# Optimization experiments

Measured on AMD Instinct MI355X. Metric: run time of the kernel, lower is better.

The kernel has to match this reference:

```python
import jax, jax.numpy as jnp
import numpy as np

N = 100000   # num nodes
F = 256      # feat_data dim == args.feat_dim (required by concat shapes)
D = 32       # fixed neighbor count per node
B = 8192     # batch of node indices
NEG = 10     # neg_sample_size (hard-coded in module)


def setup_inputs() -> dict:
    key = jax.random.key(0)
    ks = jax.random.split(key, 9)
    feat_data = jax.random.normal(ks[0], (N, F), dtype=jnp.float32)
    # self.feats[i] = [degrees[i]] * feat_dim
    degrees = jax.random.randint(ks[1], (N,), 1, 64).astype(jnp.float32)
    feats = jnp.tile(degrees[:, None], (1, F))
    W1 = jax.random.normal(ks[2], (F, 2 * F), dtype=jnp.float32) * 0.02
    b1 = jnp.zeros((F,), dtype=jnp.float32)
    W2 = jax.random.normal(ks[3], (F, 2 * F), dtype=jnp.float32) * 0.02
    b2 = jnp.zeros((F,), dtype=jnp.float32)
    adj = jax.random.randint(ks[4], (N, D), 0, N)          # adj_lists as fixed-degree matrix
    inputs1 = jax.random.randint(ks[5], (B,), 0, N)
    inputs2 = jax.random.randint(ks[6], (B,), 0, N)
    neg = jax.random.randint(ks[7], (NEG,), 0, N)           # unigram neg samples (passed in for determinism)
    return dict(feat_data=feat_data, feats=feats, W1=W1, b1=b1, W2=W2, b2=b2,
                adj=adj, inputs1=inputs1, inputs2=inputs2, neg=neg)


def _aggregate(feat_data, feats, W1, b1, W2, b2, adj, nodes):
    # aggregator(nodes): for each node, agg_one_hop over its neighbors, summed.
    node_feats = feat_data[nodes]                            # [B, F]
    nb = adj[nodes]                                          # [B, D]
    # agg_one_hop: linear1(concat(feat_data[nb], feats[nb]))
    nb_in = jnp.concatenate([feat_data[nb], feats[nb]], axis=-1)   # [B, D, 2F]
    emb = jnp.einsum('bdk,ok->bdo', nb_in, W1) + b1          # [B, D, F]
    neighbor_emb = emb.sum(axis=1)                           # [B, F] (bias summed D times, as in torch)
    final_in = jnp.concatenate([node_feats, neighbor_emb], axis=-1)  # [B, 2F]
    return final_in @ W2.T + b2                              # [B, F]


def _l2norm(x):
    # F.normalize(x, dim=1), eps=1e-12
    n = jnp.linalg.norm(x, axis=1, keepdims=True)
    return x / jnp.maximum(n, 1e-12)


def reference(feat_data, feats, W1, b1, W2, b2, adj, inputs1, inputs2, neg):
    out1 = _l2norm(_aggregate(feat_data, feats, W1, b1, W2, b2, adj, inputs1))
    out2 = _l2norm(_aggregate(feat_data, feats, W1, b1, W2, b2, adj, inputs2))
    neg_out = _l2norm(_aggregate(feat_data, feats, W1, b1, W2, b2, adj, neg))
    return (out1, out2, neg_out)
```

## Files before the change

### kernel.cpp

```cpp
#include <hip/hip_runtime.h>
#include <hip/hip_bf16.h>

#define FDIM 256
#define K2   512
#define DNB  32
#define TM   32
#define NMAX 100000
#define TMAX 20480

typedef __attribute__((ext_vector_type(8))) short bf16x8;
typedef __attribute__((ext_vector_type(8))) unsigned short u16x8;
typedef __attribute__((ext_vector_type(4))) float f32x4;

__device__ __align__(16) unsigned short g_FDb[(size_t)NMAX * FDIM];
__device__ __align__(16) unsigned short g_Xb[(size_t)TMAX * K2];
__device__ float g_degb[NMAX];
__device__ float g_Sdegb[TMAX];
__device__ __align__(16) unsigned short g_Wc[FDIM * K2];
__device__ float g_c2[FDIM];
__device__ float g_c3[FDIM];

__device__ __forceinline__ unsigned short f2bf(float f) {
    __hip_bfloat16 h = __float2bfloat16(f);
    return *reinterpret_cast<unsigned short*>(&h);
}
__device__ __forceinline__ float bf2f(unsigned short u) {
    return __uint_as_float(((unsigned)u) << 16);
}

__global__ __launch_bounds__(256) void build16(const float* __restrict__ fd,
                                               unsigned short* tab_p, int N) {
    unsigned short* tab = tab_p ? tab_p : g_FDb;

    size_t tidg = (size_t)blockIdx.x * 256 + threadIdx.x;
    size_t nthr = (size_t)gridDim.x * 256;
    size_t total8 = (size_t)N * (FDIM / 8);
    const float4* in4 = (const float4*)fd;
    u16x8* out8 = (u16x8*)tab;

    size_t i = tidg;
    for (; i + 3 * nthr < total8; i += 4 * nthr) {
        float4 a[4], b[4];
        #pragma unroll
        for (int j = 0; j < 4; ++j) {
            size_t g = i + (size_t)j * nthr;
            a[j] = in4[2 * g];
            b[j] = in4[2 * g + 1];
        }
        #pragma unroll
        for (int j = 0; j < 4; ++j) {
            size_t g = i + (size_t)j * nthr;
            u16x8 o;
            o[0] = f2bf(a[j].x); o[1] = f2bf(a[j].y);
            o[2] = f2bf(a[j].z); o[3] = f2bf(a[j].w);
            o[4] = f2bf(b[j].x); o[5] = f2bf(b[j].y);
            o[6] = f2bf(b[j].z); o[7] = f2bf(b[j].w);
            out8[g] = o;
        }
    }
    for (; i < total8; i += nthr) {
        float4 a = in4[2 * i], b = in4[2 * i + 1];
        u16x8 o;
        o[0] = f2bf(a.x); o[1] = f2bf(a.y); o[2] = f2bf(a.z); o[3] = f2bf(a.w);
        o[4] = f2bf(b.x); o[5] = f2bf(b.y); o[6] = f2bf(b.z); o[7] = f2bf(b.w);
        out8[i] = o;
    }
}

__global__ __launch_bounds__(256) void prep_w(const float* __restrict__ W1,
                                              const float* __restrict__ W2,
                                              const float* __restrict__ b1,
                                              const float* __restrict__ b2,
                                              const float* __restrict__ feats,
                                              float* deg_p,
                                              float Dmul, int N) {
    float* deg = deg_p ? deg_p : g_degb;
    __shared__ float w2s[FDIM];
    __shared__ float rv[4], ru[4];
    int o = blockIdx.x, tid = threadIdx.x;

    for (size_t n = (size_t)o * 256 + tid; n < (size_t)N; n += 65536)
        deg[n] = feats[n * FDIM];

    w2s[tid] = W2[(size_t)o * K2 + FDIM + tid];
    __syncthreads();

    const float* w1a = W1 + tid;
    const float* w1b = W1 + FDIM + tid;
    float acc0 = 0.f, acc1 = 0.f;
    for (int j = 0; j < FDIM; j += 8) {
        float r0[8], r1[8];
        #pragma unroll
        for (int u = 0; u < 8; ++u) {
            r0[u] = w1a[(size_t)(j + u) * K2];
            r1[u] = w1b[(size_t)(j + u) * K2];
        }
        #pragma unroll
        for (int u = 0; u < 8; ++u) {
            acc0 = fmaf(w2s[j + u], r0[u], acc0);
            acc1 = fmaf(w2s[j + u], r1[u], acc1);
        }
    }
    g_Wc[(size_t)o * K2 + FDIM + tid] = f2bf(acc0);
    g_Wc[(size_t)o * K2 + tid]        = f2bf(W2[(size_t)o * K2 + tid]);

    float v = acc1;
    float u = b1[tid] * w2s[tid];
    #pragma unroll
    for (int s = 32; s; s >>= 1) { v += __shfl_down(v, s); u += __shfl_down(u, s); }
    if ((tid & 63) == 0) { rv[tid >> 6] = v; ru[tid >> 6] = u; }
    __syncthreads();
    if (tid == 0) {
        g_c2[o] = rv[0] + rv[1] + rv[2] + rv[3];
        g_c3[o] = b2[o] + Dmul * (ru[0] + ru[1] + ru[2] + ru[3]);
    }
}

__global__ __launch_bounds__(256, 6) void gather(
    const unsigned short* tab_p, const float* deg_p,
    const int* __restrict__ adj,
    const int* __restrict__ in1, int B1,
    const int* __restrict__ in2, int B2,
    const int* __restrict__ neg, int total,
    unsigned short* X_p, float* Sdeg_p)
{
    const unsigned short* tab = tab_p ? tab_p : g_FDb;
    const float* deg = deg_p ? deg_p : g_degb;
    unsigned short* X = X_p ? X_p : g_Xb;
    float* Sdeg = Sdeg_p ? Sdeg_p : g_Sdegb;

    int wave = threadIdx.x >> 6, lane = threadIdx.x & 63;
    int t = blockIdx.x * 4 + wave;
    if (t >= total) return;
    int node = (t < B1) ? in1[t] : ((t < B1 + B2) ? in2[t - B1] : neg[t - B1 - B2]);

    int idx = 0; float dg = 0.f;
    if (lane < DNB) {
        idx = adj[(size_t)node * DNB + lane];
        dg = deg[idx];
    }
    #pragma unroll
    for (int s = 16; s; s >>= 1) dg += __shfl_down(dg, s);
    if (lane == 0) Sdeg[t] = dg;

    ushort4 nf = *(const ushort4*)(tab + (size_t)node * FDIM + lane * 4);
    *(ushort4*)(X + (size_t)t * K2 + lane * 4) = nf;

    float a0 = 0.f, a1 = 0.f, a2 = 0.f, a3 = 0.f;
    #pragma unroll
    for (int d = 0; d < DNB; d += 8) {
        ushort4 v[8];
        #pragma unroll
        for (int u = 0; u < 8; ++u) {
            int nb = __shfl(idx, d + u);
            v[u] = *(const ushort4*)(tab + (size_t)nb * FDIM + lane * 4);
        }
        #pragma unroll
        for (int u = 0; u < 8; ++u) {
            a0 += bf2f(v[u].x);
            a1 += bf2f(v[u].y);
            a2 += bf2f(v[u].z);
            a3 += bf2f(v[u].w);
        }
    }
    *(ushort4*)(X + (size_t)t * K2 + FDIM + lane * 4) =
        make_ushort4(f2bf(a0), f2bf(a1), f2bf(a2), f2bf(a3));
}

__global__ __launch_bounds__(256, 4) void gemm_norm(const unsigned short* X_p,
                                                    const float* Sdeg_p,
                                                    float* __restrict__ out, int total)
{
    const unsigned short* X = X_p ? X_p : g_Xb;
    const float* SdegG = Sdeg_p ? Sdeg_p : g_Sdegb;

    __shared__ __align__(16) char lds[TM * 1024];
    __shared__ float Sdeg[TM];

    int tid = threadIdx.x, wave = tid >> 6, lane = tid & 63;
    int base = blockIdx.x * TM;

    if (tid < TM) {
        int t = base + tid;
        Sdeg[tid] = (t < total) ? SdegG[t] : 0.f;
    }
    #pragma unroll
    for (int i = 0; i < 8; ++i) {
        int row = wave * 8 + i;
        int t = base + row;
        bf16x8 v = {0, 0, 0, 0, 0, 0, 0, 0};
        if (t < total) v = *(const bf16x8*)(X + (size_t)t * K2 + lane * 8);
        *(bf16x8*)(lds + row * 1024 + ((lane * 16) ^ ((row & 7) << 4))) = v;
    }
    __syncthreads();

    int l15 = lane & 15, lg = lane >> 4;
    int swzA = (l15 & 7) << 4;
    f32x4 acc[2][4];
    #pragma unroll
    for (int mt = 0; mt < 2; ++mt)
        #pragma unroll
        for (int nt = 0; nt < 4; ++nt) acc[mt][nt] = (f32x4){0.f, 0.f, 0.f, 0.f};

    const char* pA0 = lds + (size_t)l15 * 1024;
    const char* pA1 = lds + (size_t)(16 + l15) * 1024;
    const unsigned short* wcB = g_Wc + (size_t)(wave * 64 + l15) * K2 + lg * 8;

    #pragma unroll 4
    for (int kk = 0; kk < K2; kk += 32) {
        int kb = kk * 2 + lg * 16;
        bf16x8 a0 = *(const bf16x8*)(pA0 + (kb ^ swzA));
        bf16x8 a1 = *(const bf16x8*)(pA1 + (kb ^ swzA));
        #pragma unroll
        for (int nt = 0; nt < 4; ++nt) {
            bf16x8 b = *(const bf16x8*)(wcB + (size_t)nt * 16 * K2 + kk);
            acc[0][nt] = __builtin_amdgcn_mfma_f32_16x16x32_bf16(a0, b, acc[0][nt], 0, 0, 0);
            acc[1][nt] = __builtin_amdgcn_mfma_f32_16x16x32_bf16(a1, b, acc[1][nt], 0, 0, 0);
        }
    }
    __syncthreads();

    float* outf = (float*)lds;
    #pragma unroll
    for (int mt = 0; mt < 2; ++mt)
        #pragma unroll
        for (int nt = 0; nt < 4; ++nt)
            #pragma unroll
            for (int r = 0; r < 4; ++r) {
                int row = mt * 16 + lg * 4 + r;
                int col = wave * 64 + nt * 16 + l15;
                outf[row * 256 + col] = acc[mt][nt][r];
            }
    __syncthreads();

    float4 c2v = *(const float4*)(g_c2 + lane * 4);
    float4 c3v = *(const float4*)(g_c3 + lane * 4);
    for (int r = 0; r < 8; ++r) {
        int row = wave * 8 + r;
        int t = base + row;
        if (t >= total) break;
        float sd = Sdeg[row];
        float4 v = *(float4*)(outf + row * 256 + lane * 4);
        v.x += sd * c2v.x + c3v.x;
        v.y += sd * c2v.y + c3v.y;
        v.z += sd * c2v.z + c3v.z;
        v.w += sd * c2v.w + c3v.w;
        float ss = v.x * v.x + v.y * v.y + v.z * v.z + v.w * v.w;
        #pragma unroll
        for (int s = 32; s; s >>= 1) ss += __shfl_xor(ss, s);
        float inv = 1.0f / fmaxf(sqrtf(ss), 1e-12f);
        v.x *= inv; v.y *= inv; v.z *= inv; v.w *= inv;
        *(float4*)(out + (size_t)t * FDIM + lane * 4) = v;
    }
}

extern "C" void kernel_launch(void* const* d_in, const int* in_sizes, int n_in,
                              void* d_out, int out_size, void* d_ws, size_t ws_size,
                              hipStream_t stream) {
    const float* feat_data = (const float*)d_in[0];
    const float* feats     = (const float*)d_in[1];
    const float* W1        = (const float*)d_in[2];
    const float* b1        = (const float*)d_in[3];
    const float* W2        = (const float*)d_in[4];
    const float* b2        = (const float*)d_in[5];
    const int*   adj       = (const int*)d_in[6];
    const int*   in1       = (const int*)d_in[7];
    const int*   in2       = (const int*)d_in[8];
    const int*   neg       = (const int*)d_in[9];

    int B1 = in_sizes[7];
    int B2 = in_sizes[8];
    int Bn = in_sizes[9];
    int N  = in_sizes[0] / FDIM;
    int D  = in_sizes[6] / N;

    float* out = (float*)d_out;
    int total = B1 + B2 + Bn;

    size_t off = 0;
    auto take = [&](size_t bytes) { size_t o = off; off = (off + bytes + 255) & ~(size_t)255; return o; };
    size_t tab_o  = take((size_t)N * FDIM * 2);
    size_t x_o    = take((size_t)total * K2 * 2);
    size_t deg_o  = take((size_t)N * 4);
    size_t sdeg_o = take((size_t)total * 4);
    bool usews = (ws_size >= off);

    char* wsb = (char*)d_ws;
    unsigned short* tab = usews ? (unsigned short*)(wsb + tab_o) : nullptr;
    unsigned short* X   = usews ? (unsigned short*)(wsb + x_o)   : nullptr;
    float* deg  = usews ? (float*)(wsb + deg_o)  : nullptr;
    float* Sdeg = usews ? (float*)(wsb + sdeg_o) : nullptr;

    build16<<<2048, 256, 0, stream>>>(feat_data, tab, N);
    prep_w<<<FDIM, 256, 0, stream>>>(W1, W2, b1, b2, feats, deg, (float)D, N);
    gather<<<(total + 3) / 4, 256, 0, stream>>>(tab, deg, adj, in1, B1, in2, B2,
                                                neg, total, X, Sdeg);
    gemm_norm<<<(total + TM - 1) / TM, 256, 0, stream>>>(X, Sdeg, out, total);
}
```

Measured before the change: 112.4 us.

## Fuse gather with GEMM+normalize and merge bf16 conversion with weight prep

Merges the feature-table bf16 conversion and the weight-folding prep into one launch by splitting blocks by index, and adds nontemporal loads and stores to the conversion. Fuses the neighbor gather directly into the MFMA GEMM + L2-normalize kernel with 16-row tiles kept in LDS. This removes the intermediate X/Sdeg buffers and their global round trip, and drops two launches. In exchange, each block's GEMM tile halves, so the W reads from L2 are reused across fewer rows.

```diff
diff --git a/kernel.cpp b/kernel.cpp
--- a/kernel.cpp
+++ b/kernel.cpp
@@ -4,18 +4,15 @@
 #define FDIM 256
 #define K2   512
 #define DNB  32
-#define TM   32
 #define NMAX 100000
-#define TMAX 20480
+#define CONVB 2048
 
 typedef __attribute__((ext_vector_type(8))) short bf16x8;
-typedef __attribute__((ext_vector_type(8))) unsigned short u16x8;
 typedef __attribute__((ext_vector_type(4))) float f32x4;
+typedef __attribute__((ext_vector_type(4))) unsigned int u32x4;
 
 __device__ __align__(16) unsigned short g_FDb[(size_t)NMAX * FDIM];
-__device__ __align__(16) unsigned short g_Xb[(size_t)TMAX * K2];
 __device__ float g_degb[NMAX];
-__device__ float g_Sdegb[TMAX];
 __device__ __align__(16) unsigned short g_Wc[FDIM * K2];
 __device__ float g_c2[FDIM];
 __device__ float g_c3[FDIM];
@@ -27,57 +24,68 @@
 __device__ __forceinline__ float bf2f(unsigned short u) {
     return __uint_as_float(((unsigned)u) << 16);
 }
-
-__global__ __launch_bounds__(256) void build16(const float* __restrict__ fd,
-                                               unsigned short* tab_p, int N) {
+__device__ __forceinline__ unsigned int pack2(float lo, float hi) {
+    return (unsigned int)f2bf(lo) | ((unsigned int)f2bf(hi) << 16);
+}
+
+__global__ __launch_bounds__(256) void build_prep(
+    const float* __restrict__ fd,
+    const float* __restrict__ feats,
+    const float* __restrict__ W1,
+    const float* __restrict__ W2,
+    const float* __restrict__ b1,
+    const float* __restrict__ b2,
+    float Dmul, int N,
+    unsigned short* tab_p, float* deg_p)
+{
     unsigned short* tab = tab_p ? tab_p : g_FDb;
-
-    size_t tidg = (size_t)blockIdx.x * 256 + threadIdx.x;
-    size_t nthr = (size_t)gridDim.x * 256;
-    size_t total8 = (size_t)N * (FDIM / 8);
-    const float4* in4 = (const float4*)fd;
-    u16x8* out8 = (u16x8*)tab;
-
-    size_t i = tidg;
-    for (; i + 3 * nthr < total8; i += 4 * nthr) {
-        float4 a[4], b[4];
-        #pragma unroll
-        for (int j = 0; j < 4; ++j) {
-            size_t g = i + (size_t)j * nthr;
-            a[j] = in4[2 * g];
-            b[j] = in4[2 * g + 1];
-        }
-        #pragma unroll
-        for (int j = 0; j < 4; ++j) {
-            size_t g = i + (size_t)j * nthr;
-            u16x8 o;
-            o[0] = f2bf(a[j].x); o[1] = f2bf(a[j].y);
-            o[2] = f2bf(a[j].z); o[3] = f2bf(a[j].w);
-            o[4] = f2bf(b[j].x); o[5] = f2bf(b[j].y);
-            o[6] = f2bf(b[j].z); o[7] = f2bf(b[j].w);
-            out8[g] = o;
-        }
-    }
-    for (; i < total8; i += nthr) {
-        float4 a = in4[2 * i], b = in4[2 * i + 1];
-        u16x8 o;
-        o[0] = f2bf(a.x); o[1] = f2bf(a.y); o[2] = f2bf(a.z); o[3] = f2bf(a.w);
-        o[4] = f2bf(b.x); o[5] = f2bf(b.y); o[6] = f2bf(b.z); o[7] = f2bf(b.w);
-        out8[i] = o;
-    }
-}
-
-__global__ __launch_bounds__(256) void prep_w(const float* __restrict__ W1,
-                                              const float* __restrict__ W2,
-                                              const float* __restrict__ b1,
-                                              const float* __restrict__ b2,
-                                              const float* __restrict__ feats,
-                                              float* deg_p,
-                                              float Dmul, int N) {
     float* deg = deg_p ? deg_p : g_degb;
+    int bid = blockIdx.x;
+    int tid = threadIdx.x;
+
+    if (bid >= 256) {
+        size_t tidg = (size_t)(bid - 256) * 256 + tid;
+        size_t nthr = (size_t)CONVB * 256;
+        size_t total8 = (size_t)N * (FDIM / 8);
+        const f32x4* in4 = (const f32x4*)fd;
+        u32x4* out8 = (u32x4*)tab;
+
+        size_t i = tidg;
+        for (; i + 3 * nthr < total8; i += 4 * nthr) {
+            f32x4 a[4], b[4];
+            #pragma unroll
+            for (int j = 0; j < 4; ++j) {
+                size_t g = i + (size_t)j * nthr;
+                a[j] = __builtin_nontemporal_load(in4 + 2 * g);
+                b[j] = __builtin_nontemporal_load(in4 + 2 * g + 1);
+            }
+            #pragma unroll
+            for (int j = 0; j < 4; ++j) {
+                size_t g = i + (size_t)j * nthr;
+                u32x4 o;
+                o.x = pack2(a[j].x, a[j].y);
+                o.y = pack2(a[j].z, a[j].w);
+                o.z = pack2(b[j].x, b[j].y);
+                o.w = pack2(b[j].z, b[j].w);
+                __builtin_nontemporal_store(o, out8 + g);
+            }
+        }
+        for (; i < total8; i += nthr) {
+            f32x4 a = __builtin_nontemporal_load(in4 + 2 * i);
+            f32x4 b = __builtin_nontemporal_load(in4 + 2 * i + 1);
+            u32x4 o;
+            o.x = pack2(a.x, a.y);
+            o.y = pack2(a.z, a.w);
+            o.z = pack2(b.x, b.y);
+            o.w = pack2(b.z, b.w);
+            __builtin_nontemporal_store(o, out8 + i);
+        }
+        return;
+    }
+
     __shared__ float w2s[FDIM];
     __shared__ float rv[4], ru[4];
-    int o = blockIdx.x, tid = threadIdx.x;
+    int o = bid;
 
     for (size_t n = (size_t)o * 256 + tid; n < (size_t)N; n += 65536)
         deg[n] = feats[n * FDIM];
@@ -116,127 +124,110 @@
     }
 }
 
-__global__ __launch_bounds__(256, 6) void gather(
+__global__ __launch_bounds__(256, 6) void gg_norm(
     const unsigned short* tab_p, const float* deg_p,
     const int* __restrict__ adj,
     const int* __restrict__ in1, int B1,
     const int* __restrict__ in2, int B2,
     const int* __restrict__ neg, int total,
-    unsigned short* X_p, float* Sdeg_p)
+    float* __restrict__ out)
 {
     const unsigned short* tab = tab_p ? tab_p : g_FDb;
     const float* deg = deg_p ? deg_p : g_degb;
-    unsigned short* X = X_p ? X_p : g_Xb;
-    float* Sdeg = Sdeg_p ? Sdeg_p : g_Sdegb;
-
-    int wave = threadIdx.x >> 6, lane = threadIdx.x & 63;
-    int t = blockIdx.x * 4 + wave;
-    if (t >= total) return;
-    int node = (t < B1) ? in1[t] : ((t < B1 + B2) ? in2[t - B1] : neg[t - B1 - B2]);
-
-    int idx = 0; float dg = 0.f;
-    if (lane < DNB) {
-        idx = adj[(size_t)node * DNB + lane];
-        dg = deg[idx];
-    }
-    #pragma unroll
-    for (int s = 16; s; s >>= 1) dg += __shfl_down(dg, s);
-    if (lane == 0) Sdeg[t] = dg;
-
-    ushort4 nf = *(const ushort4*)(tab + (size_t)node * FDIM + lane * 4);
-    *(ushort4*)(X + (size_t)t * K2 + lane * 4) = nf;
-
-    float a0 = 0.f, a1 = 0.f, a2 = 0.f, a3 = 0.f;
-    #pragma unroll
-    for (int d = 0; d < DNB; d += 8) {
-        ushort4 v[8];
-        #pragma unroll
-        for (int u = 0; u < 8; ++u) {
-            int nb = __shfl(idx, d + u);
-            v[u] = *(const ushort4*)(tab + (size_t)nb * FDIM + lane * 4);
-        }
-        #pragma unroll
-        for (int u = 0; u < 8; ++u) {
-            a0 += bf2f(v[u].x);
-            a1 += bf2f(v[u].y);
-            a2 += bf2f(v[u].z);
-            a3 += bf2f(v[u].w);
-        }
-    }
-    *(ushort4*)(X + (size_t)t * K2 + FDIM + lane * 4) =
-        make_ushort4(f2bf(a0), f2bf(a1), f2bf(a2), f2bf(a3));
-}
-
-__global__ __launch_bounds__(256, 4) void gemm_norm(const unsigned short* X_p,
-                                                    const float* Sdeg_p,
-                                                    float* __restrict__ out, int total)
-{
-    const unsigned short* X = X_p ? X_p : g_Xb;
-    const float* SdegG = Sdeg_p ? Sdeg_p : g_Sdegb;
-
-    __shared__ __align__(16) char lds[TM * 1024];
-    __shared__ float Sdeg[TM];
+
+    __shared__ __align__(16) char lds[16 * 1024];
+    __shared__ float Sdeg[16];
 
     int tid = threadIdx.x, wave = tid >> 6, lane = tid & 63;
-    int base = blockIdx.x * TM;
-
-    if (tid < TM) {
-        int t = base + tid;
-        Sdeg[tid] = (t < total) ? SdegG[t] : 0.f;
-    }
-    #pragma unroll
-    for (int i = 0; i < 8; ++i) {
-        int row = wave * 8 + i;
+    int base = blockIdx.x * 16;
+
+    #pragma unroll
+    for (int i = 0; i < 4; ++i) {
+        int row = wave * 4 + i;
         int t = base + row;
-        bf16x8 v = {0, 0, 0, 0, 0, 0, 0, 0};
-        if (t < total) v = *(const bf16x8*)(X + (size_t)t * K2 + lane * 8);
-        *(bf16x8*)(lds + row * 1024 + ((lane * 16) ^ ((row & 7) << 4))) = v;
+        char* rowp = lds + row * 1024;
+        int swz = (row & 7) << 4;
+        int boff = (lane * 8) ^ swz;
+        if (t >= total) {
+            ushort4 z = make_ushort4(0, 0, 0, 0);
+            *(ushort4*)(rowp + boff) = z;
+            *(ushort4*)(rowp + 512 + boff) = z;
+            if (lane == 0) Sdeg[row] = 0.f;
+            continue;
+        }
+        int node = (t < B1) ? in1[t] : ((t < B1 + B2) ? in2[t - B1] : neg[t - B1 - B2]);
+
+        int idx = 0; float dg = 0.f;
+        if (lane < DNB) {
+            idx = adj[(size_t)node * DNB + lane];
+            dg = deg[idx];
+        }
+        #pragma unroll
+        for (int s = 16; s; s >>= 1) dg += __shfl_down(dg, s);
+        if (lane == 0) Sdeg[row] = dg;
+
+        ushort4 nf = *(const ushort4*)(tab + (size_t)node * FDIM + lane * 4);
+        *(ushort4*)(rowp + boff) = nf;
+
+        float a0 = 0.f, a1 = 0.f, a2 = 0.f, a3 = 0.f;
+        #pragma unroll
+        for (int d = 0; d < DNB; d += 8) {
+            ushort4 v[8];
+            #pragma unroll
+            for (int u = 0; u < 8; ++u) {
+                int nb = __shfl(idx, d + u);
+                v[u] = *(const ushort4*)(tab + (size_t)nb * FDIM + lane * 4);
+            }
+            #pragma unroll
+            for (int u = 0; u < 8; ++u) {
+                a0 += bf2f(v[u].x);
+                a1 += bf2f(v[u].y);
+                a2 += bf2f(v[u].z);
+                a3 += bf2f(v[u].w);
+            }
+        }
+        *(ushort4*)(rowp + 512 + boff) =
+            make_ushort4(f2bf(a0), f2bf(a1), f2bf(a2), f2bf(a3));
     }
     __syncthreads();
 
     int l15 = lane & 15, lg = lane >> 4;
     int swzA = (l15 & 7) << 4;
-    f32x4 acc[2][4];
-    #pragma unroll
-    for (int mt = 0; mt < 2; ++mt)
-        #pragma unroll
-        for (int nt = 0; nt < 4; ++nt) acc[mt][nt] = (f32x4){0.f, 0.f, 0.f, 0.f};
-
-    const char* pA0 = lds + (size_t)l15 * 1024;
-    const char* pA1 = lds + (size_t)(16 + l15) * 1024;
+    f32x4 acc[4];
+    #pragma unroll
+    for (int nt = 0; nt < 4; ++nt) acc[nt] = (f32x4){0.f, 0.f, 0.f, 0.f};
+
+    const char* pA = lds + (size_t)l15 * 1024;
     const unsigned short* wcB = g_Wc + (size_t)(wave * 64 + l15) * K2 + lg * 8;
 
     #pragma unroll 4
     for (int kk = 0; kk < K2; kk += 32) {
         int kb = kk * 2 + lg * 16;
-        bf16x8 a0 = *(const bf16x8*)(pA0 + (kb ^ swzA));
-        bf16x8 a1 = *(const bf16x8*)(pA1 + (kb ^ swzA));
+        bf16x8 a0 = *(const bf16x8*)(pA + (kb ^ swzA));
         #pragma unroll
         for (int nt = 0; nt < 4; ++nt) {
             bf16x8 b = *(const bf16x8*)(wcB + (size_t)nt * 16 * K2 + kk);
-            acc[0][nt] = __builtin_amdgcn_mfma_f32_16x16x32_bf16(a0, b, acc[0][nt], 0, 0, 0);
-            acc[1][nt] = __builtin_amdgcn_mfma_f32_16x16x32_bf16(a1, b, acc[1][nt], 0, 0, 0);
+            acc[nt] = __builtin_amdgcn_mfma_f32_16x16x32_bf16(a0, b, acc[nt], 0, 0, 0);
         }
     }
     __syncthreads();
 
     float* outf = (float*)lds;
     #pragma unroll
-    for (int mt = 0; mt < 2; ++mt)
-        #pragma unroll
-        for (int nt = 0; nt < 4; ++nt)
-            #pragma unroll
-            for (int r = 0; r < 4; ++r) {
-                int row = mt * 16 + lg * 4 + r;
-                int col = wave * 64 + nt * 16 + l15;
-                outf[row * 256 + col] = acc[mt][nt][r];
-            }
+    for (int nt = 0; nt < 4; ++nt)
+        #pragma unroll
+        for (int r = 0; r < 4; ++r) {
+            int row = lg * 4 + r;
+            int col = wave * 64 + nt * 16 + l15;
+            outf[row * 256 + col] = acc[nt][r];
+        }
     __syncthreads();
 
     float4 c2v = *(const float4*)(g_c2 + lane * 4);
     float4 c3v = *(const float4*)(g_c3 + lane * 4);
-    for (int r = 0; r < 8; ++r) {
-        int row = wave * 8 + r;
+    #pragma unroll
+    for (int r = 0; r < 4; ++r) {
+        int row = wave * 4 + r;
         int t = base + row;
         if (t >= total) break;
         float sd = Sdeg[row];
@@ -277,23 +268,14 @@
     float* out = (float*)d_out;
     int total = B1 + B2 + Bn;
 
-    size_t off = 0;
-    auto take = [&](size_t bytes) { size_t o = off; off = (off + bytes + 255) & ~(size_t)255; return o; };
-    size_t tab_o  = take((size_t)N * FDIM * 2);
-    size_t x_o    = take((size_t)total * K2 * 2);
-    size_t deg_o  = take((size_t)N * 4);
-    size_t sdeg_o = take((size_t)total * 4);
-    bool usews = (ws_size >= off);
-
-    char* wsb = (char*)d_ws;
-    unsigned short* tab = usews ? (unsigned short*)(wsb + tab_o) : nullptr;
-    unsigned short* X   = usews ? (unsigned short*)(wsb + x_o)   : nullptr;
-    float* deg  = usews ? (float*)(wsb + deg_o)  : nullptr;
-    float* Sdeg = usews ? (float*)(wsb + sdeg_o) : nullptr;
-
-    build16<<<2048, 256, 0, stream>>>(feat_data, tab, N);
-    prep_w<<<FDIM, 256, 0, stream>>>(W1, W2, b1, b2, feats, deg, (float)D, N);
-    gather<<<(total + 3) / 4, 256, 0, stream>>>(tab, deg, adj, in1, B1, in2, B2,
-                                                neg, total, X, Sdeg);
-    gemm_norm<<<(total + TM - 1) / TM, 256, 0, stream>>>(X, Sdeg, out, total);
-}
+    size_t tab_bytes = (size_t)N * FDIM * 2;
+    size_t need = ((tab_bytes + 255) & ~(size_t)255) + (size_t)N * 4;
+    bool usews = (ws_size >= need);
+    unsigned short* tab = usews ? (unsigned short*)d_ws : nullptr;
+    float* deg = usews ? (float*)((char*)d_ws + ((tab_bytes + 255) & ~(size_t)255)) : nullptr;
+
+    build_prep<<<256 + CONVB, 256, 0, stream>>>(feat_data, feats, W1, W2, b1, b2,
+                                                (float)D, N, tab, deg);
+    gg_norm<<<(total + 15) / 16, 256, 0, stream>>>(tab, deg, adj, in1, B1,
+                                                   in2, B2, neg, total, out);
+}
```

New measurement: 117.3 us. 1.04x slower.
